# Kernel optimization log

Hardware: AMD Instinct MI355X
Metric: run time of the kernel (lower is better)

The kernel has to match this reference:

```python
import jax, jax.numpy as jnp
import numpy as np

DIM = 192; HEADS = 6; HDIM = DIM // HEADS
WS = (2, 8, 8); SS = (1, 4, 4)
B, D, H, W = 2, 8, 64, 64
N = WS[0] * WS[1] * WS[2]          # 128 tokens per window
MLP_H = int(DIM * 2.0)
SCALE = HDIM ** -0.5


def _rel_pos_index_np():
    wd, wh, ww = WS
    coords = np.stack(np.meshgrid(np.arange(wd), np.arange(wh), np.arange(ww), indexing='ij'))
    cf = coords.reshape(3, -1)                      # (3, N)
    rel = (cf[:, :, None] - cf[:, None, :]).transpose(1, 2, 0)  # (N, N, 3)
    rel[..., 0] += wd - 1; rel[..., 1] += wh - 1; rel[..., 2] += ww - 1
    rel[..., 0] *= (2 * wh - 1) * (2 * ww - 1)
    rel[..., 1] *= (2 * ww - 1)
    return rel.sum(-1).astype(np.int32)            # (N, N)


def _compute_mask_np():
    wd, wh, ww = WS; sd, sh, sw = SS
    Dp = -(-D // wd) * wd; Hp = -(-H // wh) * wh; Wp = -(-W // ww) * ww
    img = np.zeros((1, Dp, Hp, Wp, 1), np.float32)
    cnt = 0
    for ds in (slice(0, -wd), slice(-wd, -sd), slice(-sd, None)):
        for hs in (slice(0, -wh), slice(-wh, -sh), slice(-sh, None)):
            for vs in (slice(0, -ww), slice(-ww, -sw), slice(-sw, None)):
                img[:, ds, hs, vs, :] = cnt; cnt += 1
    m = img.reshape(1, Dp // wd, wd, Hp // wh, wh, Wp // ww, ww, 1)
    m = m.transpose(0, 1, 3, 5, 2, 4, 6, 7).reshape(-1, N)       # (nW, N)
    am = m[:, None, :] - m[:, :, None]
    return np.where(am != 0, -100.0, 0.0).astype(np.float32)     # (nW, N, N)


def setup_inputs() -> dict:
    key = jax.random.key(0)
    ks = jax.random.split(key, 6)
    f = lambda k, s: (jax.random.normal(k, s, jnp.float32) * 0.02)
    n_bias = (2 * WS[0] - 1) * (2 * WS[1] - 1) * (2 * WS[2] - 1)  # 675
    return dict(
        x=jax.random.normal(ks[0], (B, D, H, W, DIM), jnp.float32),
        mask_matrix=jnp.asarray(_compute_mask_np()),
        rel_pos_index=jnp.asarray(_rel_pos_index_np()),
        gamma1=jnp.ones((DIM,), jnp.float32), beta1=jnp.zeros((DIM,), jnp.float32),
        w_qkv=f(ks[1], (3 * DIM, DIM)), b_qkv=jnp.zeros((3 * DIM,), jnp.float32),
        rpb=f(ks[2], (n_bias, HEADS)),
        w_proj=f(ks[3], (DIM, DIM)), b_proj=jnp.zeros((DIM,), jnp.float32),
        gamma2=jnp.ones((DIM,), jnp.float32), beta2=jnp.zeros((DIM,), jnp.float32),
        w_fc1=f(ks[4], (MLP_H, DIM)), b_fc1=jnp.zeros((MLP_H,), jnp.float32),
        w_fc2=f(ks[5], (DIM, MLP_H)), b_fc2=jnp.zeros((DIM,), jnp.float32),
    )


def _ln(x, g, b, eps=1e-5):
    mu = x.mean(-1, keepdims=True)
    var = ((x - mu) ** 2).mean(-1, keepdims=True)
    return (x - mu) * jax.lax.rsqrt(var + eps) * g + b


def _stl(x, mask, rpi, gamma1, beta1, w_qkv, b_qkv, rpb, w_proj, b_proj,
         gamma2, beta2, w_fc1, b_fc1, w_fc2, b_fc2):
    wd, wh, ww = WS; sd, sh, sw = SS
    # ---- part1: LN -> pad -> roll -> window attention -> reverse ----
    xn = _ln(x, gamma1, beta1)
    pd = (wd - D % wd) % wd; ph = (wh - H % wh) % wh; pw = (ww - W % ww) % ww
    xn = jnp.pad(xn, ((0, 0), (0, pd), (0, ph), (0, pw), (0, 0)))
    Dp, Hp, Wp = D + pd, H + ph, W + pw
    sx = jnp.roll(xn, (-sd, -sh, -sw), axis=(1, 2, 3))
    # window partition -> (Bw, N, C)
    xw = sx.reshape(B, Dp // wd, wd, Hp // wh, wh, Wp // ww, ww, DIM)
    xw = xw.transpose(0, 1, 3, 5, 2, 4, 6, 7).reshape(-1, N, DIM)
    Bw = xw.shape[0]
    qkv = (xw @ w_qkv.T + b_qkv).reshape(Bw, N, 3, HEADS, HDIM).transpose(2, 0, 3, 1, 4)
    q, k, v = qkv[0] * SCALE, qkv[1], qkv[2]
    attn = jnp.einsum('bhnd,bhmd->bhnm', q, k)
    bias = rpb[rpi.reshape(-1)].reshape(N, N, HEADS).transpose(2, 0, 1)  # (H, N, N)
    attn = attn + bias[None]
    nW = mask.shape[0]
    attn = (attn.reshape(Bw // nW, nW, HEADS, N, N) + mask[None, :, None]).reshape(Bw, HEADS, N, N)
    attn = jax.nn.softmax(attn, axis=-1)
    out = jnp.einsum('bhnm,bhmd->bhnd', attn, v).transpose(0, 2, 1, 3).reshape(Bw, N, DIM)
    out = out @ w_proj.T + b_proj
    # window reverse -> un-roll -> slice
    sx = out.reshape(B, Dp // wd, Hp // wh, Wp // ww, wd, wh, ww, DIM)
    sx = sx.transpose(0, 1, 4, 2, 5, 3, 6, 7).reshape(B, Dp, Hp, Wp, DIM)
    part1 = jnp.roll(sx, (sd, sh, sw), axis=(1, 2, 3))[:, :D, :H, :W, :]
    x = x + part1
    # ---- part2: LN -> MLP (GELU, exact) ----
    y = _ln(x, gamma2, beta2)
    h = jax.nn.gelu(y @ w_fc1.T + b_fc1, approximate=False)
    return x + (h @ w_fc2.T + b_fc2)


def reference(x, mask_matrix, rel_pos_index, gamma1, beta1, w_qkv, b_qkv, rpb,
              w_proj, b_proj, gamma2, beta2, w_fc1, b_fc1, w_fc2, b_fc2):
    return _stl(x, mask_matrix, rel_pos_index, gamma1, beta1, w_qkv, b_qkv, rpb,
                w_proj, b_proj, gamma2, beta2, w_fc1, b_fc1, w_fc2, b_fc2)
```

## Files before the change

### kernel.cpp

```cpp
#include <hip/hip_runtime.h>
#include <hip/hip_bf16.h>
#include <math.h>

#define TOKS   65536
#define DIMC   192
#define NTOK   128
#define MLPH   384
#define QSCALE 0.17677669529663687f

typedef unsigned short u16;
typedef unsigned int   u32;
typedef __attribute__((ext_vector_type(8))) short bf16x8;
typedef __attribute__((ext_vector_type(4))) float f32x4;

static __device__ __forceinline__ float gelu_exact(float v) {
    return 0.5f * v * (1.f + erff(v * 0.70710678118654752f));
}
static __device__ __forceinline__ u16 f2bf(float f) {
    __hip_bfloat16 h = __float2bfloat16(f);
    return *reinterpret_cast<u16*>(&h);
}
static __device__ __forceinline__ float bf2f(u16 b) {
    u32 u = ((u32)b) << 16;
    float f;
    __builtin_memcpy(&f, &u, 4);
    return f;
}
static __device__ __forceinline__ void gl_lds16(const u16* g, u16* l) {
    __builtin_amdgcn_global_load_lds(
        (const __attribute__((address_space(1))) void*)g,
        (__attribute__((address_space(3))) void*)l, 16, 0, 0);
}

#define OFF_XW   0u
#define OFF_Q    6291456u
#define OFF_K    12582912u
#define OFF_V    18874368u
#define OFF_BF   25165824u
#define OFF_WB   25264128u

__global__ __launch_bounds__(256) void k_prep(const float* __restrict__ a,
                                              const float* __restrict__ b,
                                              const float* __restrict__ c,
                                              const float* __restrict__ d,
                                              u16* __restrict__ o,
                                              const float* __restrict__ rpb,
                                              const int* __restrict__ rpi,
                                              u16* __restrict__ biasw) {
    int bid = blockIdx.x;
    if (bid < 1152) {
        int i = bid * 256 + threadIdx.x;
        float v;
        if (i < 110592) v = a[i];
        else if (i < 147456) v = b[i - 110592];
        else if (i < 221184) v = c[i - 147456];
        else v = d[i - 221184];
        o[i] = f2bf(v);
    } else {
        int idx = (bid - 1152) * 256 + threadIdx.x;
        int h = idx >> 14;
        int n = (idx >> 7) & 127;
        int slot = idx & 127;
        int m = ((slot & 7) << 4) + (slot >> 3);
        biasw[idx] = f2bf(rpb[rpi[n * 128 + m] * 6 + h]);
    }
}

template<bool PERMUTE>
__global__ __launch_bounds__(256) void k_ln(const float* __restrict__ x,
                                            const float* __restrict__ gamma,
                                            const float* __restrict__ beta,
                                            u16* __restrict__ out) {
    int tid  = threadIdx.x;
    int lane = tid & 63, wv = tid >> 6;
    int tk = blockIdx.x * 4 + wv;
    size_t src;
    if (PERMUTE) {
        int w_all = tk >> 7, t = tk & 127;
        int b  = w_all >> 8, rem = w_all & 255;
        int di = rem >> 6, hi = (rem >> 3) & 7, wi = rem & 7;
        int qd = (di * 2 + (t >> 6) + 1) & 7;
        int qh = (hi * 8 + ((t >> 3) & 7) + 4) & 63;
        int qw = (wi * 8 + (t & 7) + 4) & 63;
        src = ((size_t)(((b * 8 + qd) * 64 + qh) * 64 + qw)) * DIMC;
    } else {
        src = (size_t)tk * DIMC;
    }
    float v0 = x[src + lane];
    float v1 = x[src + 64 + lane];
    float v2 = x[src + 128 + lane];
    float s  = v0 + v1 + v2;
    float sq = v0 * v0 + v1 * v1 + v2 * v2;
    #pragma unroll
    for (int off = 32; off; off >>= 1) {
        s  += __shfl_xor(s, off);
        sq += __shfl_xor(sq, off);
    }
    float mu   = s * (1.f / 192.f);
    float var  = sq * (1.f / 192.f) - mu * mu;
    float rstd = rsqrtf(var + 1e-5f);
    size_t o = (size_t)tk * DIMC;
    out[o + lane]       = f2bf((v0 - mu) * rstd * gamma[lane]       + beta[lane]);
    out[o + 64 + lane]  = f2bf((v1 - mu) * rstd * gamma[64 + lane]  + beta[64 + lane]);
    out[o + 128 + lane] = f2bf((v2 - mu) * rstd * gamma[128 + lane] + beta[128 + lane]);
}

template<int MODE, int KD, int NSUB>
__global__ __launch_bounds__(256) void k_mgemm(const u16* __restrict__ A,
                                               const u16* __restrict__ W,
                                               const float* __restrict__ bias,
                                               void* __restrict__ outp,
                                               const float* __restrict__ aux,
                                               u16* __restrict__ q_o,
                                               u16* __restrict__ k_o,
                                               u16* __restrict__ v_o) {
    __shared__ u16 As[2][128 * 64];
    u16*   Eu = (u16*)As;
    float* Ef = (float*)As;
    const int tid = threadIdx.x;
    const int wv = tid >> 6, l = tid & 63;
    const int l15 = l & 15, g4 = l >> 4;
    const int wm = wv >> 1, wn = wv & 1;
    const size_t m0 = (size_t)blockIdx.x * 128;
    const int nb0 = blockIdx.y * (NSUB * 64);
    const int sel = (MODE == 0) ? blockIdx.y : 0;
    const int srow = l >> 3, scol = l & 7;
    const int w = (int)(m0 >> 7);

    f32x4 acc[NSUB][4][2] = {};

    auto STAGE = [&](int b, int tcol) {
        const u16* Ab = A + m0 * KD + tcol * 64;
        #pragma unroll
        for (int j = 0; j < 4; ++j) {
            int row = (wv * 4 + j) * 8 + srow;
            int sc  = scol ^ (row & 7);
            gl_lds16(Ab + (size_t)row * KD + sc * 8, &As[b][(wv * 4 + j) * 512]);
        }
    };
    auto COMPUTE = [&](int b, int tglob) {
        #pragma unroll
        for (int kk = 0; kk < 2; ++kk) {
            bf16x8 bfr[NSUB][2];
            #pragma unroll
            for (int j = 0; j < NSUB; ++j)
                #pragma unroll
                for (int nt = 0; nt < 2; ++nt)
                    bfr[j][nt] = *(const bf16x8*)&W[(size_t)(nb0 + j * 64 + wn * 32 + nt * 16 + l15) * KD
                                                   + tglob * 64 + kk * 32 + g4 * 8];
            #pragma unroll
            for (int mt = 0; mt < 4; ++mt) {
                int row  = wm * 64 + mt * 16 + l15;
                int slot = (kk * 4 + g4) ^ (row & 7);
                bf16x8 afr = *(const bf16x8*)&As[b][row * 64 + slot * 8];
                #pragma unroll
                for (int j = 0; j < NSUB; ++j)
                    #pragma unroll
                    for (int nt = 0; nt < 2; ++nt)
                        acc[j][mt][nt] = __builtin_amdgcn_mfma_f32_16x16x32_bf16(afr, bfr[j][nt],
                                                                                 acc[j][mt][nt], 0, 0, 0);
            }
        }
    };

    constexpr int NT = KD / 64;
    STAGE(0, 0);
    __syncthreads();
    for (int t = 0; t < NT; ++t) {
        if (t + 1 < NT) STAGE((t + 1) & 1, t + 1);
        COMPUTE(t & 1, t);
        __syncthreads();
    }

    #pragma unroll
    for (int j = 0; j < NSUB; ++j) {
        const int nb = nb0 + j * 64;
        if (MODE == 0 || MODE == 2) {
            const float scl = (MODE == 0 && sel == 0) ? QSCALE : 1.f;
            #pragma unroll
            for (int mt = 0; mt < 4; ++mt)
                #pragma unroll
                for (int nt = 0; nt < 2; ++nt) {
                    int c = wn * 32 + nt * 16 + l15;
                    float bb = bias[nb + c];
                    #pragma unroll
                    for (int reg = 0; reg < 4; ++reg) {
                        int r = wm * 64 + mt * 16 + g4 * 4 + reg;
                        float v = acc[j][mt][nt][reg] + bb;
                        if (MODE == 2) v = gelu_exact(v);
                        else v *= scl;
                        int slot8 = (c >> 3) ^ ((r >> 2) & 7);
                        Eu[r * 64 + slot8 * 8 + (c & 7)] = f2bf(v);
                    }
                }
            __syncthreads();
            if (MODE == 2) {
                u16* out = (u16*)outp;
                #pragma unroll
                for (int p = 0; p < 4; ++p) {
                    int cid = p * 256 + tid;
                    int r = cid >> 3, jj = cid & 7;
                    int slot8 = jj ^ ((r >> 2) & 7);
                    bf16x8 vv = *(const bf16x8*)&Eu[r * 64 + slot8 * 8];
                    *(bf16x8*)&out[(m0 + r) * MLPH + nb + jj * 8] = vv;
                }
            } else if (sel < 2) {
                u16* dst = sel ? k_o : q_o;
                #pragma unroll
                for (int p = 0; p < 4; ++p) {
                    int cid = p * 256 + tid;
                    int r = cid >> 3, jj = cid & 7;
                    int c0 = jj * 8;
                    int slot8 = jj ^ ((r >> 2) & 7);
                    bf16x8 vv = *(const bf16x8*)&Eu[r * 64 + slot8 * 8];
                    size_t b9 = (size_t)(w * 6 + j * 2 + (c0 >> 5)) * 4096;
                    *(bf16x8*)&dst[b9 + (size_t)r * 32 + (c0 & 31)] = vv;
                }
            } else {
                #pragma unroll
                for (int p = 0; p < 4; ++p) {
                    int cid = p * 256 + tid;
                    int c = cid >> 4, jt = cid & 15;
                    int t0 = jt * 8;
                    u16 tmp[8];
                    #pragma unroll
                    for (int i = 0; i < 8; ++i) {
                        int r = t0 + i;
                        int slot8 = (c >> 3) ^ ((r >> 2) & 7);
                        tmp[i] = Eu[r * 64 + slot8 * 8 + (c & 7)];
                    }
                    size_t b9 = (size_t)(w * 6 + j * 2 + (c >> 5)) * 4096;
                    *(bf16x8*)&v_o[b9 + (size_t)(c & 31) * 128 + t0] = *(bf16x8*)tmp;
                }
            }
            __syncthreads();
        } else {
            #pragma unroll
            for (int mt = 0; mt < 4; ++mt)
                #pragma unroll
                for (int nt = 0; nt < 2; ++nt) {
                    int c = wn * 32 + nt * 16 + l15;
                    float bb = bias[nb + c];
                    #pragma unroll
                    for (int reg = 0; reg < 4; ++reg) {
                        int r = wm * 64 + mt * 16 + g4 * 4 + reg;
                        int swz = (c >> 2) ^ ((r >> 2) & 3);
                        Ef[r * 64 + swz * 4 + (c & 3)] = acc[j][mt][nt][reg] + bb;
                    }
                }
            __syncthreads();
            float* out = (float*)outp;
            #pragma unroll
            for (int p = 0; p < 8; ++p) {
                int cid = p * 256 + tid;
                int r = cid >> 4, jj = cid & 15;
                int swz = jj ^ ((r >> 2) & 3);
                float4 vv = *(const float4*)&Ef[r * 64 + swz * 4];
                size_t drow;
                if (MODE == 1) {
                    int m = (int)m0 + r;
                    int w_all = m >> 7, tt = m & 127;
                    int b  = w_all >> 8, rem = w_all & 255;
                    int di = rem >> 6, hi = (rem >> 3) & 7, wi = rem & 7;
                    int qd = (di * 2 + (tt >> 6) + 1) & 7;
                    int qh = (hi * 8 + ((tt >> 3) & 7) + 4) & 63;
                    int qw = (wi * 8 + (tt & 7) + 4) & 63;
                    drow = (size_t)(((b * 8 + qd) * 64 + qh) * 64 + qw) * DIMC;
                } else {
                    drow = (m0 + r) * DIMC;
                }
                float4 ax = *(const float4*)&aux[drow + nb + jj * 4];
                vv.x += ax.x; vv.y += ax.y; vv.z += ax.z; vv.w += ax.w;
                *(float4*)&out[drow + nb + jj * 4] = vv;
            }
            __syncthreads();
        }
    }
}

__global__ __launch_bounds__(256) void k_attn(const u16* __restrict__ qb,
                                              const u16* __restrict__ kb,
                                              const u16* __restrict__ vb,
                                              const u16* __restrict__ biasw,
                                              u16* __restrict__ attn_out) {
    __shared__ u16 Pl[4][32 * 128];
    u16* Ou = (u16*)Pl;
    int wh = blockIdx.x;
    int w_all = wh / 6, head = wh - w_all * 6;
    int wl = w_all & 255;
    int tid = threadIdx.x;
    int wv = tid >> 6, l = tid & 63;
    int l15 = l & 15, g4 = l >> 4;
    size_t base = (size_t)wh * 4096;
    const u16* qg = qb + base;
    const u16* kg = kb + base;
    const u16* vg = vb + base;
    int rowb = wv * 32;

    bf16x8 qa[2];
    #pragma unroll
    for (int rt = 0; rt < 2; ++rt)
        qa[rt] = *(const bf16x8*)&qg[(size_t)(rowb + rt * 16 + l15) * 32 + g4 * 8];

    f32x4 s[2][8] = {};
    #pragma unroll
    for (int ct = 0; ct < 8; ++ct) {
        bf16x8 kf = *(const bf16x8*)&kg[(size_t)(ct * 16 + l15) * 32 + g4 * 8];
        s[0][ct] = __builtin_amdgcn_mfma_f32_16x16x32_bf16(qa[0], kf, s[0][ct], 0, 0, 0);
        s[1][ct] = __builtin_amdgcn_mfma_f32_16x16x32_bf16(qa[1], kf, s[1][ct], 0, 0, 0);
    }

    int di = wl >> 6, hi = (wl >> 3) & 7, wi = wl & 7;
    auto rcode = [&](int t) {
        int d = di * 2 + (t >> 6);
        int h = hi * 8 + ((t >> 3) & 7);
        int w = wi * 8 + (t & 7);
        int rd = (d < 6) ? 0 : (d < 7 ? 1 : 2);
        int rh = (h < 56) ? 0 : (h < 60 ? 1 : 2);
        int rw = (w < 56) ? 0 : (w < 60 ? 1 : 2);
        return rd * 9 + rh * 3 + rw;
    };
    int rm[8];
    #pragma unroll
    for (int ct = 0; ct < 8; ++ct) rm[ct] = rcode(ct * 16 + l15);

    const u16* bh = biasw + (size_t)head * 16384;
    #pragma unroll
    for (int rt = 0; rt < 2; ++rt)
        #pragma unroll
        for (int reg = 0; reg < 4; ++reg) {
            int n = rowb + rt * 16 + g4 * 4 + reg;
            int rn = rcode(n);
            bf16x8 bv = *(const bf16x8*)&bh[(size_t)n * 128 + l15 * 8];
            #pragma unroll
            for (int ct = 0; ct < 8; ++ct) {
                float mval = (rn == rm[ct]) ? 0.f : -100.f;
                s[rt][ct][reg] += bf2f((u16)bv[ct]) + mval;
            }
        }

    u16* Pw = Pl[wv];
    #pragma unroll
    for (int rt = 0; rt < 2; ++rt)
        #pragma unroll
        for (int reg = 0; reg < 4; ++reg) {
            float mx = -1e30f;
            #pragma unroll
            for (int ct = 0; ct < 8; ++ct) mx = fmaxf(mx, s[rt][ct][reg]);
            #pragma unroll
            for (int off = 1; off < 16; off <<= 1) mx = fmaxf(mx, __shfl_xor(mx, off));
            float sum = 0.f;
            #pragma unroll
            for (int ct = 0; ct < 8; ++ct) {
                float p = __expf(s[rt][ct][reg] - mx);
                s[rt][ct][reg] = p; sum += p;
            }
            #pragma unroll
            for (int off = 1; off < 16; off <<= 1) sum += __shfl_xor(sum, off);
            float inv = 1.f / sum;
            int nloc = rt * 16 + g4 * 4 + reg;
            int sw = ((nloc >> 2) & 3) << 4;
            #pragma unroll
            for (int ct = 0; ct < 8; ++ct) {
                int m = ct * 16 + l15;
                Pw[nloc * 128 + (m ^ sw)] = f2bf(s[rt][ct][reg] * inv);
            }
        }
    __syncthreads();

    f32x4 o[2][2] = {};
    #pragma unroll
    for (int kt = 0; kt < 4; ++kt) {
        bf16x8 vf[2];
        #pragma unroll
        for (int dt = 0; dt < 2; ++dt)
            vf[dt] = *(const bf16x8*)&vg[(size_t)(dt * 16 + l15) * 128 + kt * 32 + g4 * 8];
        #pragma unroll
        for (int rt = 0; rt < 2; ++rt) {
            int nloc = rt * 16 + l15;
            int sw = ((nloc >> 2) & 3) << 4;
            int m8 = kt * 32 + g4 * 8;
            bf16x8 pa = *(const bf16x8*)&Pw[nloc * 128 + (m8 ^ sw)];
            #pragma unroll
            for (int dt = 0; dt < 2; ++dt)
                o[rt][dt] = __builtin_amdgcn_mfma_f32_16x16x32_bf16(pa, vf[dt], o[rt][dt], 0, 0, 0);
        }
    }

    __syncthreads();
    #pragma unroll
    for (int rt = 0; rt < 2; ++rt)
        #pragma unroll
        for (int dt = 0; dt < 2; ++dt)
            #pragma unroll
            for (int reg = 0; reg < 4; ++reg) {
                int r = rowb + rt * 16 + g4 * 4 + reg;
                int c = dt * 16 + l15;
                int slot8 = (c >> 3) ^ ((r >> 2) & 3);
                Ou[r * 32 + slot8 * 8 + (c & 7)] = f2bf(o[rt][dt][reg]);
            }
    __syncthreads();
    #pragma unroll
    for (int p = 0; p < 2; ++p) {
        int cid = p * 256 + tid;
        int r = cid >> 2, j = cid & 3;
        int slot8 = j ^ ((r >> 2) & 3);
        bf16x8 vv = *(const bf16x8*)&Ou[r * 32 + slot8 * 8];
        *(bf16x8*)&attn_out[((size_t)(w_all * 128 + r)) * DIMC + head * 32 + j * 8] = vv;
    }
}

extern "C" void kernel_launch(void* const* d_in, const int* in_sizes, int n_in,
                              void* d_out, int out_size, void* d_ws, size_t ws_size,
                              hipStream_t stream) {
    const float* x      = (const float*)d_in[0];
    const int*   rpi    = (const int*)d_in[2];
    const float* gamma1 = (const float*)d_in[3];
    const float* beta1  = (const float*)d_in[4];
    const float* w_qkv  = (const float*)d_in[5];
    const float* b_qkv  = (const float*)d_in[6];
    const float* rpb    = (const float*)d_in[7];
    const float* w_proj = (const float*)d_in[8];
    const float* b_proj = (const float*)d_in[9];
    const float* gamma2 = (const float*)d_in[10];
    const float* beta2  = (const float*)d_in[11];
    const float* w_fc1  = (const float*)d_in[12];
    const float* b_fc1  = (const float*)d_in[13];
    const float* w_fc2  = (const float*)d_in[14];
    const float* b_fc2  = (const float*)d_in[15];

    float* ws    = (float*)d_ws;
    u16*   xwu   = (u16*)(ws + OFF_XW);
    u16*   qbu   = (u16*)(ws + OFF_Q);
    u16*   kbu   = (u16*)(ws + OFF_K);
    u16*   vbu   = (u16*)(ws + OFF_V);
    u16*   hbu   = (u16*)(ws + OFF_Q);
    u16*   ybu   = (u16*)(ws + OFF_V);
    u16*   biasw = (u16*)(ws + OFF_BF);
    u16*   wb    = (u16*)(ws + OFF_WB);
    float* xres  = (float*)d_out;

    const u16* wqkv_b  = wb;
    const u16* wproj_b = wb + 110592;
    const u16* wfc1_b  = wb + 147456;
    const u16* wfc2_b  = wb + 221184;

    k_prep<<<1536, 256, 0, stream>>>(w_qkv, w_proj, w_fc1, w_fc2, wb, rpb, rpi, biasw);
    k_ln<true><<<16384, 256, 0, stream>>>(x, gamma1, beta1, xwu);
    k_mgemm<0, 192, 3><<<dim3(512, 3), 256, 0, stream>>>(xwu, wqkv_b, b_qkv, nullptr, nullptr,
                                                         qbu, kbu, vbu);
    k_attn<<<3072, 256, 0, stream>>>(qbu, kbu, vbu, biasw, xwu);
    k_mgemm<1, 192, 1><<<dim3(512, 3), 256, 0, stream>>>(xwu, wproj_b, b_proj, xres, x,
                                                         nullptr, nullptr, nullptr);
    k_ln<false><<<16384, 256, 0, stream>>>(xres, gamma2, beta2, ybu);
    k_mgemm<2, 192, 3><<<dim3(512, 2), 256, 0, stream>>>(ybu, wfc1_b, b_fc1, hbu, nullptr,
                                                         nullptr, nullptr, nullptr);
    k_mgemm<3, 384, 3><<<dim3(512, 1), 256, 0, stream>>>(hbu, wfc2_b, b_fc2, xres, xres,
                                                         nullptr, nullptr, nullptr);
}
```

Measured before the change: 242.3 us.

## Shrink GEMM block tile to one 64-col subtile with 512 threads

Replaces the multi-subtile GEMM blocks (up to 192 output columns per block, 256 threads) with 512-thread blocks that each compute a single 128x64 output tile, launching more blocks along N. This lowers per-thread accumulator count and raises occupancy and parallelism. In exchange, each A tile is loaded from global memory once per 64-column slice instead of being reused across three subtiles, increasing A traffic.

```diff
diff --git a/kernel.cpp b/kernel.cpp
--- a/kernel.cpp
+++ b/kernel.cpp
@@ -105,8 +105,8 @@
     out[o + 128 + lane] = f2bf((v2 - mu) * rstd * gamma[128 + lane] + beta[128 + lane]);
 }
 
-template<int MODE, int KD, int NSUB>
-__global__ __launch_bounds__(256) void k_mgemm(const u16* __restrict__ A,
+template<int MODE, int KD>
+__global__ __launch_bounds__(512) void k_mgemm(const u16* __restrict__ A,
                                                const u16* __restrict__ W,
                                                const float* __restrict__ bias,
                                                void* __restrict__ outp,
@@ -122,43 +122,38 @@
     const int l15 = l & 15, g4 = l >> 4;
     const int wm = wv >> 1, wn = wv & 1;
     const size_t m0 = (size_t)blockIdx.x * 128;
-    const int nb0 = blockIdx.y * (NSUB * 64);
-    const int sel = (MODE == 0) ? blockIdx.y : 0;
+    const int n0 = blockIdx.y * 64;
     const int srow = l >> 3, scol = l & 7;
     const int w = (int)(m0 >> 7);
 
-    f32x4 acc[NSUB][4][2] = {};
+    f32x4 acc[2][2] = {};
 
     auto STAGE = [&](int b, int tcol) {
         const u16* Ab = A + m0 * KD + tcol * 64;
         #pragma unroll
-        for (int j = 0; j < 4; ++j) {
-            int row = (wv * 4 + j) * 8 + srow;
+        for (int j = 0; j < 2; ++j) {
+            int row = (wv * 2 + j) * 8 + srow;
             int sc  = scol ^ (row & 7);
-            gl_lds16(Ab + (size_t)row * KD + sc * 8, &As[b][(wv * 4 + j) * 512]);
+            gl_lds16(Ab + (size_t)row * KD + sc * 8, &As[b][(wv * 2 + j) * 512]);
         }
     };
     auto COMPUTE = [&](int b, int tglob) {
         #pragma unroll
         for (int kk = 0; kk < 2; ++kk) {
-            bf16x8 bfr[NSUB][2];
-            #pragma unroll
-            for (int j = 0; j < NSUB; ++j)
-                #pragma unroll
-                for (int nt = 0; nt < 2; ++nt)
-                    bfr[j][nt] = *(const bf16x8*)&W[(size_t)(nb0 + j * 64 + wn * 32 + nt * 16 + l15) * KD
-                                                   + tglob * 64 + kk * 32 + g4 * 8];
-            #pragma unroll
-            for (int mt = 0; mt < 4; ++mt) {
-                int row  = wm * 64 + mt * 16 + l15;
+            bf16x8 bfr[2];
+            #pragma unroll
+            for (int nt = 0; nt < 2; ++nt)
+                bfr[nt] = *(const bf16x8*)&W[(size_t)(n0 + wn * 32 + nt * 16 + l15) * KD
+                                             + tglob * 64 + kk * 32 + g4 * 8];
+            #pragma unroll
+            for (int mt = 0; mt < 2; ++mt) {
+                int row  = wm * 32 + mt * 16 + l15;
                 int slot = (kk * 4 + g4) ^ (row & 7);
                 bf16x8 afr = *(const bf16x8*)&As[b][row * 64 + slot * 8];
                 #pragma unroll
-                for (int j = 0; j < NSUB; ++j)
-                    #pragma unroll
-                    for (int nt = 0; nt < 2; ++nt)
-                        acc[j][mt][nt] = __builtin_amdgcn_mfma_f32_16x16x32_bf16(afr, bfr[j][nt],
-                                                                                 acc[j][mt][nt], 0, 0, 0);
+                for (int nt = 0; nt < 2; ++nt)
+                    acc[mt][nt] = __builtin_amdgcn_mfma_f32_16x16x32_bf16(afr, bfr[nt],
+                                                                          acc[mt][nt], 0, 0, 0);
             }
         }
     };
@@ -172,108 +167,105 @@
         __syncthreads();
     }
 
-    #pragma unroll
-    for (int j = 0; j < NSUB; ++j) {
-        const int nb = nb0 + j * 64;
-        if (MODE == 0 || MODE == 2) {
-            const float scl = (MODE == 0 && sel == 0) ? QSCALE : 1.f;
-            #pragma unroll
-            for (int mt = 0; mt < 4; ++mt)
+    if (MODE == 0 || MODE == 2) {
+        const int sel = (MODE == 0) ? ((n0 >= 384) ? 2 : (n0 >= 192 ? 1 : 0)) : 0;
+        const float scl = (MODE == 0 && sel == 0) ? QSCALE : 1.f;
+        #pragma unroll
+        for (int mt = 0; mt < 2; ++mt)
+            #pragma unroll
+            for (int nt = 0; nt < 2; ++nt) {
+                int c = wn * 32 + nt * 16 + l15;
+                float bb = bias[n0 + c];
                 #pragma unroll
-                for (int nt = 0; nt < 2; ++nt) {
-                    int c = wn * 32 + nt * 16 + l15;
-                    float bb = bias[nb + c];
-                    #pragma unroll
-                    for (int reg = 0; reg < 4; ++reg) {
-                        int r = wm * 64 + mt * 16 + g4 * 4 + reg;
-                        float v = acc[j][mt][nt][reg] + bb;
-                        if (MODE == 2) v = gelu_exact(v);
-                        else v *= scl;
-                        int slot8 = (c >> 3) ^ ((r >> 2) & 7);
-                        Eu[r * 64 + slot8 * 8 + (c & 7)] = f2bf(v);
-                    }
+                for (int reg = 0; reg < 4; ++reg) {
+                    int r = wm * 32 + mt * 16 + g4 * 4 + reg;
+                    float v = acc[mt][nt][reg] + bb;
+                    if (MODE == 2) v = gelu_exact(v);
+                    else v *= scl;
+                    int slot8 = (c >> 3) ^ ((r >> 2) & 7);
+                    Eu[r * 64 + slot8 * 8 + (c & 7)] = f2bf(v);
                 }
-            __syncthreads();
-            if (MODE == 2) {
-                u16* out = (u16*)outp;
+            }
+        __syncthreads();
+        if (MODE == 2) {
+            u16* out = (u16*)outp;
+            #pragma unroll
+            for (int p = 0; p < 2; ++p) {
+                int cid = p * 512 + tid;
+                int r = cid >> 3, jj = cid & 7;
+                int slot8 = jj ^ ((r >> 2) & 7);
+                bf16x8 vv = *(const bf16x8*)&Eu[r * 64 + slot8 * 8];
+                *(bf16x8*)&out[(m0 + r) * MLPH + n0 + jj * 8] = vv;
+            }
+        } else if (sel < 2) {
+            u16* dst = sel ? k_o : q_o;
+            const int hbase = (n0 - sel * 192) >> 5;
+            #pragma unroll
+            for (int p = 0; p < 2; ++p) {
+                int cid = p * 512 + tid;
+                int r = cid >> 3, jj = cid & 7;
+                int c0 = jj * 8;
+                int slot8 = jj ^ ((r >> 2) & 7);
+                bf16x8 vv = *(const bf16x8*)&Eu[r * 64 + slot8 * 8];
+                size_t b9 = (size_t)(w * 6 + hbase + (c0 >> 5)) * 4096;
+                *(bf16x8*)&dst[b9 + (size_t)r * 32 + (c0 & 31)] = vv;
+            }
+        } else {
+            const int hbase = (n0 - 384) >> 5;
+            #pragma unroll
+            for (int p = 0; p < 2; ++p) {
+                int cid = p * 512 + tid;
+                int c = cid >> 4, jt = cid & 15;
+                int t0 = jt * 8;
+                u16 tmp[8];
                 #pragma unroll
-                for (int p = 0; p < 4; ++p) {
-                    int cid = p * 256 + tid;
-                    int r = cid >> 3, jj = cid & 7;
-                    int slot8 = jj ^ ((r >> 2) & 7);
-                    bf16x8 vv = *(const bf16x8*)&Eu[r * 64 + slot8 * 8];
-                    *(bf16x8*)&out[(m0 + r) * MLPH + nb + jj * 8] = vv;
+                for (int i = 0; i < 8; ++i) {
+                    int r = t0 + i;
+                    int slot8 = (c >> 3) ^ ((r >> 2) & 7);
+                    tmp[i] = Eu[r * 64 + slot8 * 8 + (c & 7)];
                 }
-            } else if (sel < 2) {
-                u16* dst = sel ? k_o : q_o;
+                size_t b9 = (size_t)(w * 6 + hbase + (c >> 5)) * 4096;
+                *(bf16x8*)&v_o[b9 + (size_t)(c & 31) * 128 + t0] = *(bf16x8*)tmp;
+            }
+        }
+    } else {
+        #pragma unroll
+        for (int mt = 0; mt < 2; ++mt)
+            #pragma unroll
+            for (int nt = 0; nt < 2; ++nt) {
+                int c = wn * 32 + nt * 16 + l15;
+                float bb = bias[n0 + c];
                 #pragma unroll
-                for (int p = 0; p < 4; ++p) {
-                    int cid = p * 256 + tid;
-                    int r = cid >> 3, jj = cid & 7;
-                    int c0 = jj * 8;
-                    int slot8 = jj ^ ((r >> 2) & 7);
-                    bf16x8 vv = *(const bf16x8*)&Eu[r * 64 + slot8 * 8];
-                    size_t b9 = (size_t)(w * 6 + j * 2 + (c0 >> 5)) * 4096;
-                    *(bf16x8*)&dst[b9 + (size_t)r * 32 + (c0 & 31)] = vv;
+                for (int reg = 0; reg < 4; ++reg) {
+                    int r = wm * 32 + mt * 16 + g4 * 4 + reg;
+                    int swz = (c >> 2) ^ ((r >> 2) & 3);
+                    Ef[r * 64 + swz * 4 + (c & 3)] = acc[mt][nt][reg] + bb;
                 }
+            }
+        __syncthreads();
+        float* out = (float*)outp;
+        #pragma unroll
+        for (int p = 0; p < 4; ++p) {
+            int cid = p * 512 + tid;
+            int r = cid >> 4, jj = cid & 15;
+            int swz = jj ^ ((r >> 2) & 3);
+            float4 vv = *(const float4*)&Ef[r * 64 + swz * 4];
+            size_t drow;
+            if (MODE == 1) {
+                int m = (int)m0 + r;
+                int w_all = m >> 7, tt = m & 127;
+                int b  = w_all >> 8, rem = w_all & 255;
+                int di = rem >> 6, hi = (rem >> 3) & 7, wi = rem & 7;
+                int qd = (di * 2 + (tt >> 6) + 1) & 7;
+                int qh = (hi * 8 + ((tt >> 3) & 7) + 4) & 63;
+                int qw = (wi * 8 + (tt & 7) + 4) & 63;
+                drow = (size_t)(((b * 8 + qd) * 64 + qh) * 64 + qw) * DIMC;
             } else {
-                #pragma unroll
-                for (int p = 0; p < 4; ++p) {
-                    int cid = p * 256 + tid;
-                    int c = cid >> 4, jt = cid & 15;
-                    int t0 = jt * 8;
-                    u16 tmp[8];
-                    #pragma unroll
-                    for (int i = 0; i < 8; ++i) {
-                        int r = t0 + i;
-                        int slot8 = (c >> 3) ^ ((r >> 2) & 7);
-                        tmp[i] = Eu[r * 64 + slot8 * 8 + (c & 7)];
-                    }
-                    size_t b9 = (size_t)(w * 6 + j * 2 + (c >> 5)) * 4096;
-                    *(bf16x8*)&v_o[b9 + (size_t)(c & 31) * 128 + t0] = *(bf16x8*)tmp;
-                }
-            }
-            __syncthreads();
-        } else {
-            #pragma unroll
-            for (int mt = 0; mt < 4; ++mt)
-                #pragma unroll
-                for (int nt = 0; nt < 2; ++nt) {
-                    int c = wn * 32 + nt * 16 + l15;
-                    float bb = bias[nb + c];
-                    #pragma unroll
-                    for (int reg = 0; reg < 4; ++reg) {
-                        int r = wm * 64 + mt * 16 + g4 * 4 + reg;
-                        int swz = (c >> 2) ^ ((r >> 2) & 3);
-                        Ef[r * 64 + swz * 4 + (c & 3)] = acc[j][mt][nt][reg] + bb;
-                    }
-                }
-            __syncthreads();
-            float* out = (float*)outp;
-            #pragma unroll
-            for (int p = 0; p < 8; ++p) {
-                int cid = p * 256 + tid;
-                int r = cid >> 4, jj = cid & 15;
-                int swz = jj ^ ((r >> 2) & 3);
-                float4 vv = *(const float4*)&Ef[r * 64 + swz * 4];
-                size_t drow;
-                if (MODE == 1) {
-                    int m = (int)m0 + r;
-                    int w_all = m >> 7, tt = m & 127;
-                    int b  = w_all >> 8, rem = w_all & 255;
-                    int di = rem >> 6, hi = (rem >> 3) & 7, wi = rem & 7;
-                    int qd = (di * 2 + (tt >> 6) + 1) & 7;
-                    int qh = (hi * 8 + ((tt >> 3) & 7) + 4) & 63;
-                    int qw = (wi * 8 + (tt & 7) + 4) & 63;
-                    drow = (size_t)(((b * 8 + qd) * 64 + qh) * 64 + qw) * DIMC;
-                } else {
-                    drow = (m0 + r) * DIMC;
-                }
-                float4 ax = *(const float4*)&aux[drow + nb + jj * 4];
-                vv.x += ax.x; vv.y += ax.y; vv.z += ax.z; vv.w += ax.w;
-                *(float4*)&out[drow + nb + jj * 4] = vv;
-            }
-            __syncthreads();
+                drow = (m0 + r) * DIMC;
+            }
+            float4 ax = *(const float4*)&aux[drow + n0 + jj * 4];
+            vv.x += ax.x; vv.y += ax.y; vv.z += ax.z; vv.w += ax.w;
+            *(float4*)&out[drow + n0 + jj * 4] = vv;
         }
     }
 }
@@ -447,14 +439,14 @@
 
     k_prep<<<1536, 256, 0, stream>>>(w_qkv, w_proj, w_fc1, w_fc2, wb, rpb, rpi, biasw);
     k_ln<true><<<16384, 256, 0, stream>>>(x, gamma1, beta1, xwu);
-    k_mgemm<0, 192, 3><<<dim3(512, 3), 256, 0, stream>>>(xwu, wqkv_b, b_qkv, nullptr, nullptr,
-                                                         qbu, kbu, vbu);
+    k_mgemm<0, 192><<<dim3(512, 9), 512, 0, stream>>>(xwu, wqkv_b, b_qkv, nullptr, nullptr,
+                                                      qbu, kbu, vbu);
     k_attn<<<3072, 256, 0, stream>>>(qbu, kbu, vbu, biasw, xwu);
-    k_mgemm<1, 192, 1><<<dim3(512, 3), 256, 0, stream>>>(xwu, wproj_b, b_proj, xres, x,
-                                                         nullptr, nullptr, nullptr);
+    k_mgemm<1, 192><<<dim3(512, 3), 512, 0, stream>>>(xwu, wproj_b, b_proj, xres, x,
+                                                      nullptr, nullptr, nullptr);
     k_ln<false><<<16384, 256, 0, stream>>>(xres, gamma2, beta2, ybu);
-    k_mgemm<2, 192, 3><<<dim3(512, 2), 256, 0, stream>>>(ybu, wfc1_b, b_fc1, hbu, nullptr,
-                                                         nullptr, nullptr, nullptr);
-    k_mgemm<3, 384, 3><<<dim3(512, 1), 256, 0, stream>>>(hbu, wfc2_b, b_fc2, xres, xres,
-                                                         nullptr, nullptr, nullptr);
-}
+    k_mgemm<2, 192><<<dim3(512, 6), 512, 0, stream>>>(ybu, wfc1_b, b_fc1, hbu, nullptr,
+                                                      nullptr, nullptr, nullptr);
+    k_mgemm<3, 384><<<dim3(512, 3), 512, 0, stream>>>(hbu, wfc2_b, b_fc2, xres, xres,
+                                                      nullptr, nullptr, nullptr);
+}
```

New measurement: 253.7 us. +4.7%, slower.
